# Optimization experiments

Measured on AMD Instinct MI355X. Metric: run time of the kernel, lower is better.

Reference implementation:

```python
import jax, jax.numpy as jnp
import numpy as np

DIM = 768
HEADS = 12
FF = 3072
EPS = 1e-6


def setup_inputs() -> dict:
    key = jax.random.key(0)
    ks = jax.random.split(key, 12)
    B, S, D, F_ = 64, 197, DIM, FF
    s = 0.02
    inp = {
        "x": jax.random.normal(ks[0], (B, S, D), jnp.float32),
        "Wq": jax.random.normal(ks[1], (D, D), jnp.float32) * s,
        "bq": jnp.zeros((D,), jnp.float32),
        "Wk": jax.random.normal(ks[2], (D, D), jnp.float32) * s,
        "bk": jnp.zeros((D,), jnp.float32),
        "Wv": jax.random.normal(ks[3], (D, D), jnp.float32) * s,
        "bv": jnp.zeros((D,), jnp.float32),
        "Wo": jax.random.normal(ks[4], (D, D), jnp.float32) * s,
        "bo": jnp.zeros((D,), jnp.float32),
        "ln1_w": jnp.ones((D,), jnp.float32),
        "ln1_b": jnp.zeros((D,), jnp.float32),
        "W1": jax.random.normal(ks[5], (D, F_), jnp.float32) * s,
        "b1": jnp.zeros((F_,), jnp.float32),
        "W2": jax.random.normal(ks[6], (F_, D), jnp.float32) * s,
        "b2": jnp.zeros((D,), jnp.float32),
        "ln2_w": jnp.ones((D,), jnp.float32),
        "ln2_b": jnp.zeros((D,), jnp.float32),
        "mask": jnp.ones((B, S), jnp.int32),
    }
    return inp


def _layernorm(x, w, b):
    m = jnp.mean(x, axis=-1, keepdims=True)
    v = jnp.mean(jnp.square(x - m), axis=-1, keepdims=True)  # unbiased=False
    return (x - m) / jnp.sqrt(v + EPS) * w + b


def _block(x, mask_f, Wq, bq, Wk, bk, Wv, bv, Wo, bo, ln1_w, ln1_b, W1, b1, W2, b2, ln2_w, ln2_b):
    B, S, D = x.shape
    H = HEADS
    Dh = D // H
    # --- attention (pre-norm) ---
    h = _layernorm(x, ln1_w, ln1_b)
    q = (h @ Wq + bq).reshape(B, S, H, Dh).transpose(0, 2, 1, 3)
    k = (h @ Wk + bk).reshape(B, S, H, Dh).transpose(0, 2, 1, 3)
    v = (h @ Wv + bv).reshape(B, S, H, Dh).transpose(0, 2, 1, 3)
    scores = jnp.einsum("bhqd,bhkd->bhqk", q, k) / jnp.sqrt(jnp.float32(Dh))
    scores = scores - 10000.0 * (1.0 - mask_f[:, None, None, :])
    probs = jax.nn.softmax(scores, axis=-1)
    attn = jnp.einsum("bhqk,bhkd->bhqd", probs, v).transpose(0, 2, 1, 3).reshape(B, S, D)
    x = x + (attn @ Wo + bo)  # dropout = identity (eval)
    # --- FFN (pre-norm), exact erf GELU (F.gelu default) ---
    h = _layernorm(x, ln2_w, ln2_b)
    h = jax.nn.gelu(h @ W1 + b1, approximate=False)
    x = x + (h @ W2 + b2)
    return x


def reference(x, Wq, bq, Wk, bk, Wv, bv, Wo, bo, ln1_w, ln1_b, W1, b1, W2, b2, ln2_w, ln2_b, mask):
    mask_f = mask.astype(jnp.float32)
    return _block(x, mask_f, Wq, bq, Wk, bk, Wv, bv, Wo, bo, ln1_w, ln1_b, W1, b1, W2, b2, ln2_w, ln2_b)
```

## Files before the change

kernel.cpp:

```cpp
#include <hip/hip_runtime.h>
#include <stdint.h>

#define B_   64
#define S_   197
#define D_   768
#define H_   12
#define F_   3072
#define BS_  (B_ * S_)

typedef __attribute__((ext_vector_type(8))) short short8;
typedef __attribute__((ext_vector_type(4))) float f32x4;

__device__ __forceinline__ float bf2f(unsigned short h) {
    union { unsigned int u; float f; } v; v.u = ((unsigned int)h) << 16; return v.f;
}
__device__ __forceinline__ unsigned short f2bf(float f) {
    union { float f; unsigned int u; } v; v.f = f;
    unsigned int r = v.u + 0x7FFFu + ((v.u >> 16) & 1u);
    return (unsigned short)(r >> 16);
}

__device__ __forceinline__ void g2l16(const void* g, void* l) {
    __builtin_amdgcn_global_load_lds(
        (const __attribute__((address_space(1))) unsigned int*)g,
        (__attribute__((address_space(3))) unsigned int*)l, 16, 0, 0);
}

__device__ __forceinline__ float gelu_f(float c) {
    float z = fabsf(c) * 0.70710678118f;
    float t = __builtin_amdgcn_rcpf(1.f + 0.3275911f * z);
    float p = ((((1.061405429f * t - 1.453152027f) * t + 1.421413741f) * t
               - 0.284496736f) * t + 0.254829592f) * t;
    float erfv = 1.f - p * __expf(-z * z);
    erfv = c < 0.f ? -erfv : erfv;
    return 0.5f * c * (1.f + erfv);
}

__global__ __launch_bounds__(256)
void transpose_all(const float* __restrict__ Wq, const float* __restrict__ Wk,
                   const float* __restrict__ Wv, const float* __restrict__ Wo,
                   const float* __restrict__ W1, const float* __restrict__ W2,
                   const float* __restrict__ bq, const float* __restrict__ bk,
                   const float* __restrict__ bv,
                   unsigned short* __restrict__ wqkvT, unsigned short* __restrict__ woT,
                   unsigned short* __restrict__ w1T, unsigned short* __restrict__ w2T,
                   float* __restrict__ bcat) {
    int blk = blockIdx.x;
    int tx = threadIdx.x, ty = threadIdx.y;
    if (blk == 6912) {
        for (int i = ty * 32 + tx; i < 2304; i += 256)
            bcat[i] = i < 768 ? bq[i] : (i < 1536 ? bk[i - 768] : bv[i - 1536]);
        return;
    }
    const float* W; unsigned short* Wt; int K, N, rel, nx;
    if (blk < 2304) {
        int m = blk / 576; rel = blk - m * 576; K = 768; N = 768; nx = 24;
        W  = m == 0 ? Wq : m == 1 ? Wk : m == 2 ? Wv : Wo;
        Wt = m < 3 ? wqkvT + (size_t)m * 768 * 768 : woT;
    } else if (blk < 4608) {
        rel = blk - 2304; K = 768; N = 3072; nx = 96; W = W1; Wt = w1T;
    } else {
        rel = blk - 4608; K = 3072; N = 768; nx = 24; W = W2; Wt = w2T;
    }
    int n0 = (rel % nx) * 32, k0 = (rel / nx) * 32;
    __shared__ float t[32][33];
#pragma unroll
    for (int i = ty; i < 32; i += 8) t[i][tx] = W[(size_t)(k0 + i) * N + n0 + tx];
    __syncthreads();
#pragma unroll
    for (int i = ty; i < 32; i += 8) Wt[(size_t)(n0 + i) * K + k0 + tx] = f2bf(t[tx][i]);
}

__global__ __launch_bounds__(256)
void ln_kernel(const float* __restrict__ x, const float* __restrict__ w,
               const float* __restrict__ b, unsigned short* __restrict__ out) {
    int row = blockIdx.x; size_t base = (size_t)row * 768;
    int tid = threadIdx.x;
    float v0 = x[base + tid], v1 = x[base + tid + 256], v2 = x[base + tid + 512];
    float s1 = v0 + v1 + v2;
    float s2 = v0 * v0 + v1 * v1 + v2 * v2;
#pragma unroll
    for (int off = 32; off > 0; off >>= 1) { s1 += __shfl_xor(s1, off); s2 += __shfl_xor(s2, off); }
    __shared__ float sa[4], sb[4];
    int w4 = tid >> 6;
    if ((tid & 63) == 0) { sa[w4] = s1; sb[w4] = s2; }
    __syncthreads();
    s1 = sa[0] + sa[1] + sa[2] + sa[3];
    s2 = sb[0] + sb[1] + sb[2] + sb[3];
    float mean = s1 * (1.f / 768.f);
    float var  = s2 * (1.f / 768.f) - mean * mean;
    float rstd = rsqrtf(var + 1e-6f);
    out[base + tid]       = f2bf((v0 - mean) * rstd * w[tid]       + b[tid]);
    out[base + tid + 256] = f2bf((v1 - mean) * rstd * w[tid + 256] + b[tid + 256]);
    out[base + tid + 512] = f2bf((v2 - mean) * rstd * w[tid + 512] + b[tid + 512]);
}

template<int MODE>
__global__ __launch_bounds__(512, 2)
void gemm256(const unsigned short* __restrict__ A, const unsigned short* __restrict__ Bt,
             const float* __restrict__ bias, const float* __restrict__ resid,
             void* __restrict__ out, int M, int N, int K) {
    __shared__ unsigned short As[2][256 * 64];
    __shared__ unsigned short Bs[2][256 * 64];
    const int tid = threadIdx.x;
    const int l = tid & 63, wid = tid >> 6;
    const int lr = l & 15, lg = l >> 4;
    const int wr = wid >> 2, wc = wid & 3;

    const int nMt = gridDim.y;
    const int nwg = gridDim.x * gridDim.y;
    const int orig = blockIdx.x + gridDim.x * blockIdx.y;
    const int q8 = nwg >> 3, r8 = nwg & 7;
    const int xcd = orig & 7, idx = orig >> 3;
    const int wgid = (xcd < r8 ? xcd * (q8 + 1) : r8 * (q8 + 1) + (xcd - r8) * q8) + idx;
    const int bm0 = (wgid % nMt) * 256;
    const int bn0 = (wgid / nMt) * 256;

    const int srow_lo = l >> 3;
    const int slb = (l & 7) ^ (l >> 3);

    auto stageChunk = [&](int buf, int kt, int c) {
        int ca = c & 3;
        int row = ca * 64 + wid * 8 + srow_lo;
        unsigned short* dst;
        const unsigned short* src;
        if (c < 4) {
            int gr = bm0 + row; gr = gr < M ? gr : M - 1;
            src = A + (size_t)gr * K + kt * 64 + slb * 8;
            dst = &As[buf][(ca * 512 + wid * 64) * 8];
        } else {
            int gr = bn0 + row;
            src = Bt + (size_t)gr * K + kt * 64 + slb * 8;
            dst = &Bs[buf][(ca * 512 + wid * 64) * 8];
        }
        g2l16(src, dst);
    };

    f32x4 acc[8][4];
#pragma unroll
    for (int i = 0; i < 8; ++i)
#pragma unroll
        for (int j = 0; j < 4; ++j) acc[i][j] = (f32x4){0.f, 0.f, 0.f, 0.f};

    const int NK = K >> 6;
#pragma unroll
    for (int c = 0; c < 8; ++c) stageChunk(0, 0, c);
    asm volatile("s_waitcnt vmcnt(0)" ::: "memory");
    __builtin_amdgcn_s_barrier();

    const int rsw = lr & 7;
    for (int kt = 0; kt < NK; ++kt) {
        const int buf = kt & 1;
        const bool pf = (kt + 1 < NK);
        short8 bfr[4][2];
#pragma unroll
        for (int q = 0; q < 4; ++q) {
            if (q == 0) {
#pragma unroll
                for (int nt = 0; nt < 4; ++nt)
#pragma unroll
                    for (int kk = 0; kk < 2; ++kk)
                        bfr[nt][kk] = *(const short8*)&Bs[buf][(wc * 64 + nt * 16 + lr) * 64 +
                                                              (((kk * 4 + lg) ^ rsw) * 8)];
            }
            short8 af[2][2];
#pragma unroll
            for (int tmt = 0; tmt < 2; ++tmt)
#pragma unroll
                for (int kk = 0; kk < 2; ++kk)
                    af[tmt][kk] = *(const short8*)&As[buf][(wr * 128 + (q * 2 + tmt) * 16 + lr) * 64 +
                                                          (((kk * 4 + lg) ^ rsw) * 8)];
            if (pf && q == 0) {
#pragma unroll
                for (int c = 0; c < 4; ++c) stageChunk(buf ^ 1, kt + 1, c);
            }
            if (pf && q == 1) {
#pragma unroll
                for (int c = 4; c < 8; ++c) stageChunk(buf ^ 1, kt + 1, c);
            }
            asm volatile("s_waitcnt lgkmcnt(0)" ::: "memory");
            __builtin_amdgcn_sched_barrier(0);
            __builtin_amdgcn_s_setprio(1);
#pragma unroll
            for (int tmt = 0; tmt < 2; ++tmt)
#pragma unroll
                for (int nt = 0; nt < 4; ++nt)
#pragma unroll
                    for (int kk = 0; kk < 2; ++kk)
                        acc[q * 2 + tmt][nt] = __builtin_amdgcn_mfma_f32_16x16x32_bf16(
                            af[tmt][kk], bfr[nt][kk], acc[q * 2 + tmt][nt], 0, 0, 0);
            __builtin_amdgcn_s_setprio(0);
        }
        if (pf) {
            asm volatile("s_waitcnt vmcnt(0)" ::: "memory");
            __builtin_amdgcn_s_barrier();
        }
    }

#pragma unroll
    for (int mt = 0; mt < 8; ++mt)
#pragma unroll
        for (int nt = 0; nt < 4; ++nt)
#pragma unroll
            for (int r = 0; r < 4; ++r) {
                int gm = bm0 + wr * 128 + mt * 16 + lg * 4 + r;
                int gn = bn0 + wc * 64 + nt * 16 + lr;
                if (gm < M) {
                    float c = acc[mt][nt][r] + bias[gn];
                    if (MODE == 0) {
                        if (gn < 768) c *= 0.125f;
                        ((unsigned short*)out)[(size_t)gm * N + gn] = f2bf(c);
                    } else if (MODE == 1) {
                        ((float*)out)[(size_t)gm * N + gn] = c + resid[(size_t)gm * N + gn];
                    } else {
                        ((unsigned short*)out)[(size_t)gm * N + gn] = f2bf(gelu_f(c));
                    }
                }
            }
}

__global__ __launch_bounds__(256)
void attn_mfma(const unsigned short* __restrict__ qkv, const int* __restrict__ mask,
               unsigned short* __restrict__ ctx) {
    __shared__ unsigned short Ks[208 * 64];
    __shared__ unsigned short Vt[64 * 256];
    __shared__ unsigned short Psl[4][16 * 40];
    __shared__ float maskadj[224];
    const int bh = blockIdx.x, b = bh / 12, h = bh - b * 12;
    const int tid = threadIdx.x, l = tid & 63, w = tid >> 6;
    const int lr = l & 15, lg = l >> 4;
    const unsigned short* Qg = qkv + (size_t)b * 197 * 2304 + h * 64;
    const unsigned short* Kg = Qg + 768;
    const unsigned short* Vg = Qg + 1536;

    if (tid < 224)
        maskadj[tid] = tid < 197 ? -10000.f * (1.f - (float)mask[b * 197 + tid]) : -1e30f;

    for (int c = w; c < 26; c += 4) {
        int row = c * 8 + (l >> 3);
        int rc = row < 197 ? row : 196;
        int blk = (l & 7) ^ (row & 7);
        g2l16(Kg + (size_t)rc * 2304 + blk * 8, &Ks[c * 8 * 64]);
    }
    {
        int jj = tid >> 3, db = tid & 7;
#pragma unroll
        for (int it = 0; it < 7; ++it) {
            int j = it * 32 + jj;
            short8 v = (short8){0, 0, 0, 0, 0, 0, 0, 0};
            if (j < 197) v = *(const short8*)(Vg + (size_t)j * 2304 + db * 8);
#pragma unroll
            for (int e = 0; e < 8; ++e) {
                int d = db * 8 + e;
                Vt[d * 256 + (((j >> 3) ^ (d & 7)) * 8) + (j & 7)] = (unsigned short)v[e];
            }
        }
    }
    __syncthreads();

    for (int t = w; t < 13; t += 4) {
        const int q0 = t * 16;
        int qr = q0 + lr; qr = qr < 197 ? qr : 196;
        const short8 qf0 = *(const short8*)(Qg + (size_t)qr * 2304 + lg * 8);
        const short8 qf1 = *(const short8*)(Qg + (size_t)qr * 2304 + 32 + lg * 8);

        f32x4 sc[13];
#pragma unroll
        for (int kt = 0; kt < 13; ++kt) {
            const int krow = kt * 16 + lr;
            const short8 kf0 = *(const short8*)&Ks[krow * 64 + ((lg ^ (lr & 7)) * 8)];
            const short8 kf1 = *(const short8*)&Ks[krow * 64 + (((4 + lg) ^ (lr & 7)) * 8)];
            f32x4 a = (f32x4){0.f, 0.f, 0.f, 0.f};
            a = __builtin_amdgcn_mfma_f32_16x16x32_bf16(qf0, kf0, a, 0, 0, 0);
            a = __builtin_amdgcn_mfma_f32_16x16x32_bf16(qf1, kf1, a, 0, 0, 0);
            sc[kt] = a;
        }
        float mx[4] = {-1e30f, -1e30f, -1e30f, -1e30f};
#pragma unroll
        for (int kt = 0; kt < 13; ++kt) {
            float ma = maskadj[kt * 16 + lr];
#pragma unroll
            for (int r = 0; r < 4; ++r) {
                sc[kt][r] += ma;
                mx[r] = fmaxf(mx[r], sc[kt][r]);
            }
        }
#pragma unroll
        for (int r = 0; r < 4; ++r) {
            mx[r] = fmaxf(mx[r], __shfl_xor(mx[r], 1));
            mx[r] = fmaxf(mx[r], __shfl_xor(mx[r], 2));
            mx[r] = fmaxf(mx[r], __shfl_xor(mx[r], 4));
            mx[r] = fmaxf(mx[r], __shfl_xor(mx[r], 8));
        }
        float sm[4] = {0.f, 0.f, 0.f, 0.f};
#pragma unroll
        for (int kt = 0; kt < 13; ++kt)
#pragma unroll
            for (int r = 0; r < 4; ++r) {
                float p = __expf(sc[kt][r] - mx[r]);
                sc[kt][r] = p;
                sm[r] += p;
            }
#pragma unroll
        for (int r = 0; r < 4; ++r) {
            sm[r] += __shfl_xor(sm[r], 1);
            sm[r] += __shfl_xor(sm[r], 2);
            sm[r] += __shfl_xor(sm[r], 4);
            sm[r] += __shfl_xor(sm[r], 8);
            sm[r] = 1.f / sm[r];
        }
        f32x4 ao[4];
#pragma unroll
        for (int dt = 0; dt < 4; ++dt) ao[dt] = (f32x4){0.f, 0.f, 0.f, 0.f};
        unsigned short* Pw = &Psl[w][0];
#pragma unroll
        for (int ks = 0; ks < 7; ++ks) {
#pragma unroll
            for (int tl = 0; tl < 2; ++tl) {
                const int kt = ks * 2 + tl;
#pragma unroll
                for (int r = 0; r < 4; ++r) {
                    unsigned short pv = 0;
                    if (kt < 13) pv = f2bf(sc[kt][r] * sm[r]);
                    Pw[(lg * 4 + r) * 40 + tl * 16 + lr] = pv;
                }
            }
            const short8 pf = *(const short8*)&Pw[lr * 40 + lg * 8];
#pragma unroll
            for (int dt = 0; dt < 4; ++dt) {
                const int drow = dt * 16 + lr;
                const short8 vf = *(const short8*)&Vt[drow * 256 + (((4 * ks + lg) ^ (lr & 7)) * 8)];
                ao[dt] = __builtin_amdgcn_mfma_f32_16x16x32_bf16(vf, pf, ao[dt], 0, 0, 0);
            }
        }
        const int q = q0 + lr;
        if (q < 197) {
            unsigned short* crow = ctx + ((size_t)b * 197 + q) * 768 + h * 64;
#pragma unroll
            for (int dt = 0; dt < 4; ++dt) {
                union { unsigned short u[4]; uint2 v; } pk;
#pragma unroll
                for (int r = 0; r < 4; ++r) pk.u[r] = f2bf(ao[dt][r]);
                *(uint2*)(crow + dt * 16 + lg * 4) = pk.v;
            }
        }
    }
}

extern "C" void kernel_launch(void* const* d_in, const int* in_sizes, int n_in,
                              void* d_out, int out_size, void* d_ws, size_t ws_size,
                              hipStream_t stream) {
    const float* x    = (const float*)d_in[0];
    const float* Wq   = (const float*)d_in[1];
    const float* bq   = (const float*)d_in[2];
    const float* Wk   = (const float*)d_in[3];
    const float* bk   = (const float*)d_in[4];
    const float* Wv   = (const float*)d_in[5];
    const float* bv   = (const float*)d_in[6];
    const float* Wo   = (const float*)d_in[7];
    const float* bo   = (const float*)d_in[8];
    const float* ln1w = (const float*)d_in[9];
    const float* ln1b = (const float*)d_in[10];
    const float* W1   = (const float*)d_in[11];
    const float* b1   = (const float*)d_in[12];
    const float* W2   = (const float*)d_in[13];
    const float* b2   = (const float*)d_in[14];
    const float* ln2w = (const float*)d_in[15];
    const float* ln2b = (const float*)d_in[16];
    const int*   mask = (const int*)d_in[17];

    size_t off = 0;
    auto nxt = [&](size_t bytes) -> void* {
        void* r = (char*)d_ws + off; off += (bytes + 255) & ~(size_t)255; return r;
    };
    unsigned short* hbuf  = (unsigned short*)nxt((size_t)BS_ * 768 * 2);
    unsigned short* qkvg  = (unsigned short*)nxt((size_t)BS_ * 3072 * 2);
    unsigned short* wqkvT = (unsigned short*)nxt((size_t)2304 * 768 * 2);
    unsigned short* woT   = (unsigned short*)nxt((size_t)768 * 768 * 2);
    unsigned short* w1T   = (unsigned short*)nxt((size_t)3072 * 768 * 2);
    unsigned short* w2T   = (unsigned short*)nxt((size_t)768 * 3072 * 2);
    float*          bcat  = (float*)nxt(2304 * 4);
    unsigned short* ctx   = (unsigned short*)nxt((size_t)BS_ * 768 * 2);
    (void)ws_size; (void)in_sizes; (void)n_in; (void)out_size;

    transpose_all<<<6913, dim3(32, 8), 0, stream>>>(Wq, Wk, Wv, Wo, W1, W2, bq, bk, bv,
                                                    wqkvT, woT, w1T, w2T, bcat);
    ln_kernel<<<BS_, 256, 0, stream>>>(x, ln1w, ln1b, hbuf);
    gemm256<0><<<dim3(9, 50), 512, 0, stream>>>(hbuf, wqkvT, bcat, nullptr, qkvg, BS_, 2304, 768);
    attn_mfma<<<768, 256, 0, stream>>>(qkvg, mask, ctx);
    gemm256<1><<<dim3(3, 50), 512, 0, stream>>>(ctx, woT, bo, x, d_out, BS_, 768, 768);
    ln_kernel<<<BS_, 256, 0, stream>>>((const float*)d_out, ln2w, ln2b, hbuf);
    gemm256<2><<<dim3(12, 50), 512, 0, stream>>>(hbuf, w1T, b1, nullptr, qkvg, BS_, 3072, 768);
    gemm256<1><<<dim3(3, 50), 512, 0, stream>>>(qkvg, w2T, b2, (const float*)d_out, d_out, BS_, 768, 3072);
}
```

Measured before the change: 485.4 us.

## Shrink GEMM tile to 256x128, drop XCD remap, restructure prefetch sync

Replaces the 256x256 GEMM tile with a 256x128 tile, which halves the B shared-memory buffer and the accumulator registers and doubles the grid size for every linear layer. Removes the XCD-aware workgroup index remapping in favour of plain blockIdx mapping. Also moves the next-tile prefetch into the first sub-iteration and adds barriers around each MFMA group. The intent is better occupancy and load balance across CUs, at the cost of more global and shared traffic per FLOP, lost L2 locality from the remap, and extra barrier overhead.

```diff
diff --git a/kernel.cpp b/kernel.cpp
--- a/kernel.cpp
+++ b/kernel.cpp
@@ -97,102 +97,80 @@
 
 template<int MODE>
 __global__ __launch_bounds__(512, 2)
-void gemm256(const unsigned short* __restrict__ A, const unsigned short* __restrict__ Bt,
-             const float* __restrict__ bias, const float* __restrict__ resid,
-             void* __restrict__ out, int M, int N, int K) {
+void gemm8p(const unsigned short* __restrict__ A, const unsigned short* __restrict__ Bt,
+            const float* __restrict__ bias, const float* __restrict__ resid,
+            void* __restrict__ out, int M, int N, int K) {
     __shared__ unsigned short As[2][256 * 64];
-    __shared__ unsigned short Bs[2][256 * 64];
+    __shared__ unsigned short Bs[2][128 * 64];
     const int tid = threadIdx.x;
     const int l = tid & 63, wid = tid >> 6;
     const int lr = l & 15, lg = l >> 4;
     const int wr = wid >> 2, wc = wid & 3;
-
-    const int nMt = gridDim.y;
-    const int nwg = gridDim.x * gridDim.y;
-    const int orig = blockIdx.x + gridDim.x * blockIdx.y;
-    const int q8 = nwg >> 3, r8 = nwg & 7;
-    const int xcd = orig & 7, idx = orig >> 3;
-    const int wgid = (xcd < r8 ? xcd * (q8 + 1) : r8 * (q8 + 1) + (xcd - r8) * q8) + idx;
-    const int bm0 = (wgid % nMt) * 256;
-    const int bn0 = (wgid / nMt) * 256;
-
-    const int srow_lo = l >> 3;
-    const int slb = (l & 7) ^ (l >> 3);
-
-    auto stageChunk = [&](int buf, int kt, int c) {
-        int ca = c & 3;
-        int row = ca * 64 + wid * 8 + srow_lo;
-        unsigned short* dst;
-        const unsigned short* src;
-        if (c < 4) {
-            int gr = bm0 + row; gr = gr < M ? gr : M - 1;
-            src = A + (size_t)gr * K + kt * 64 + slb * 8;
-            dst = &As[buf][(ca * 512 + wid * 64) * 8];
-        } else {
-            int gr = bn0 + row;
-            src = Bt + (size_t)gr * K + kt * 64 + slb * 8;
-            dst = &Bs[buf][(ca * 512 + wid * 64) * 8];
-        }
-        g2l16(src, dst);
+    const int bn0 = blockIdx.x * 128, bm0 = blockIdx.y * 256;
+
+    const int srow8 = l >> 3;
+    const int slb = (l & 7) ^ srow8;
+
+    auto stageA = [&](int buf, int kt, int a) {
+        int row = a * 64 + wid * 8 + srow8;
+        int gr = bm0 + row; gr = gr < M ? gr : M - 1;
+        g2l16(A + (size_t)gr * K + kt * 64 + slb * 8, &As[buf][(a * 64 + wid * 8) * 64]);
     };
-
-    f32x4 acc[8][4];
+    auto stageB = [&](int buf, int kt, int b) {
+        int row = b * 64 + wid * 8 + srow8;
+        g2l16(Bt + (size_t)(bn0 + row) * K + kt * 64 + slb * 8, &Bs[buf][(b * 64 + wid * 8) * 64]);
+    };
+
+    f32x4 acc[8][2];
 #pragma unroll
     for (int i = 0; i < 8; ++i)
 #pragma unroll
-        for (int j = 0; j < 4; ++j) acc[i][j] = (f32x4){0.f, 0.f, 0.f, 0.f};
+        for (int j = 0; j < 2; ++j) acc[i][j] = (f32x4){0.f, 0.f, 0.f, 0.f};
 
     const int NK = K >> 6;
-#pragma unroll
-    for (int c = 0; c < 8; ++c) stageChunk(0, 0, c);
-    asm volatile("s_waitcnt vmcnt(0)" ::: "memory");
-    __builtin_amdgcn_s_barrier();
-
-    const int rsw = lr & 7;
-    for (int kt = 0; kt < NK; ++kt) {
-        const int buf = kt & 1;
-        const bool pf = (kt + 1 < NK);
-        short8 bfr[4][2];
+    stageA(0, 0, 0); stageA(0, 0, 1); stageA(0, 0, 2); stageA(0, 0, 3);
+    stageB(0, 0, 0); stageB(0, 0, 1);
+
+    const int rs = lr & 7;
+    for (int t = 0; t < NK; ++t) {
+        const int buf = t & 1;
+        asm volatile("s_waitcnt vmcnt(0)" ::: "memory");
+        __builtin_amdgcn_s_barrier();
+        __builtin_amdgcn_sched_barrier(0);
+        short8 bf[2][2];
 #pragma unroll
         for (int q = 0; q < 4; ++q) {
+            short8 af[2][2];
+#pragma unroll
+            for (int mt = 0; mt < 2; ++mt)
+#pragma unroll
+                for (int kk = 0; kk < 2; ++kk)
+                    af[mt][kk] = *(const short8*)&As[buf][(wr * 128 + (q * 2 + mt) * 16 + lr) * 64 +
+                                                         (((kk * 4 + lg) ^ rs) * 8)];
             if (q == 0) {
 #pragma unroll
-                for (int nt = 0; nt < 4; ++nt)
+                for (int nt = 0; nt < 2; ++nt)
 #pragma unroll
                     for (int kk = 0; kk < 2; ++kk)
-                        bfr[nt][kk] = *(const short8*)&Bs[buf][(wc * 64 + nt * 16 + lr) * 64 +
-                                                              (((kk * 4 + lg) ^ rsw) * 8)];
-            }
-            short8 af[2][2];
-#pragma unroll
-            for (int tmt = 0; tmt < 2; ++tmt)
-#pragma unroll
-                for (int kk = 0; kk < 2; ++kk)
-                    af[tmt][kk] = *(const short8*)&As[buf][(wr * 128 + (q * 2 + tmt) * 16 + lr) * 64 +
-                                                          (((kk * 4 + lg) ^ rsw) * 8)];
-            if (pf && q == 0) {
-#pragma unroll
-                for (int c = 0; c < 4; ++c) stageChunk(buf ^ 1, kt + 1, c);
-            }
-            if (pf && q == 1) {
-#pragma unroll
-                for (int c = 4; c < 8; ++c) stageChunk(buf ^ 1, kt + 1, c);
-            }
-            asm volatile("s_waitcnt lgkmcnt(0)" ::: "memory");
-            __builtin_amdgcn_sched_barrier(0);
+                        bf[nt][kk] = *(const short8*)&Bs[buf][(wc * 32 + nt * 16 + lr) * 64 +
+                                                             (((kk * 4 + lg) ^ rs) * 8)];
+                if (t + 1 < NK) {
+                    stageA(buf ^ 1, t + 1, 0); stageA(buf ^ 1, t + 1, 1);
+                    stageA(buf ^ 1, t + 1, 2); stageA(buf ^ 1, t + 1, 3);
+                    stageB(buf ^ 1, t + 1, 0); stageB(buf ^ 1, t + 1, 1);
+                }
+            }
+            __builtin_amdgcn_s_barrier();
             __builtin_amdgcn_s_setprio(1);
 #pragma unroll
-            for (int tmt = 0; tmt < 2; ++tmt)
-#pragma unroll
-                for (int nt = 0; nt < 4; ++nt)
+            for (int mt = 0; mt < 2; ++mt)
+#pragma unroll
+                for (int nt = 0; nt < 2; ++nt)
 #pragma unroll
                     for (int kk = 0; kk < 2; ++kk)
-                        acc[q * 2 + tmt][nt] = __builtin_amdgcn_mfma_f32_16x16x32_bf16(
-                            af[tmt][kk], bfr[nt][kk], acc[q * 2 + tmt][nt], 0, 0, 0);
+                        acc[q * 2 + mt][nt] = __builtin_amdgcn_mfma_f32_16x16x32_bf16(
+                            af[mt][kk], bf[nt][kk], acc[q * 2 + mt][nt], 0, 0, 0);
             __builtin_amdgcn_s_setprio(0);
-        }
-        if (pf) {
-            asm volatile("s_waitcnt vmcnt(0)" ::: "memory");
             __builtin_amdgcn_s_barrier();
         }
     }
@@ -200,11 +178,11 @@
 #pragma unroll
     for (int mt = 0; mt < 8; ++mt)
 #pragma unroll
-        for (int nt = 0; nt < 4; ++nt)
+        for (int nt = 0; nt < 2; ++nt)
 #pragma unroll
             for (int r = 0; r < 4; ++r) {
                 int gm = bm0 + wr * 128 + mt * 16 + lg * 4 + r;
-                int gn = bn0 + wc * 64 + nt * 16 + lr;
+                int gn = bn0 + wc * 32 + nt * 16 + lr;
                 if (gm < M) {
                     float c = acc[mt][nt][r] + bias[gn];
                     if (MODE == 0) {
@@ -386,10 +364,10 @@
     transpose_all<<<6913, dim3(32, 8), 0, stream>>>(Wq, Wk, Wv, Wo, W1, W2, bq, bk, bv,
                                                     wqkvT, woT, w1T, w2T, bcat);
     ln_kernel<<<BS_, 256, 0, stream>>>(x, ln1w, ln1b, hbuf);
-    gemm256<0><<<dim3(9, 50), 512, 0, stream>>>(hbuf, wqkvT, bcat, nullptr, qkvg, BS_, 2304, 768);
+    gemm8p<0><<<dim3(18, 50), 512, 0, stream>>>(hbuf, wqkvT, bcat, nullptr, qkvg, BS_, 2304, 768);
     attn_mfma<<<768, 256, 0, stream>>>(qkvg, mask, ctx);
-    gemm256<1><<<dim3(3, 50), 512, 0, stream>>>(ctx, woT, bo, x, d_out, BS_, 768, 768);
+    gemm8p<1><<<dim3(6, 50), 512, 0, stream>>>(ctx, woT, bo, x, d_out, BS_, 768, 768);
     ln_kernel<<<BS_, 256, 0, stream>>>((const float*)d_out, ln2w, ln2b, hbuf);
-    gemm256<2><<<dim3(12, 50), 512, 0, stream>>>(hbuf, w1T, b1, nullptr, qkvg, BS_, 3072, 768);
-    gemm256<1><<<dim3(3, 50), 512, 0, stream>>>(qkvg, w2T, b2, (const float*)d_out, d_out, BS_, 768, 3072);
-}
+    gemm8p<2><<<dim3(24, 50), 512, 0, stream>>>(hbuf, w1T, b1, nullptr, qkvg, BS_, 3072, 768);
+    gemm8p<1><<<dim3(6, 50), 512, 0, stream>>>(qkvg, w2T, b2, (const float*)d_out, d_out, BS_, 768, 3072);
+}
```

Result: slower. 576.5 us (+18.8%).
